# Optimization experiments

Measured on AMD Instinct MI355X. Metric: run time of the kernel, lower is better.

Reference implementation:

```python
import jax, jax.numpy as jnp
import numpy as np
import math

EMBED_DIM = 1024
NUM_HEADS = 16
HEAD_DIM = EMBED_DIM // NUM_HEADS
BATCH = 2
SEQ = 2048


def setup_inputs() -> dict:
    key = jax.random.key(0)
    ks = jax.random.split(key, 9)
    s = 1.0 / math.sqrt(EMBED_DIM)
    return {
        "x": jax.random.normal(ks[0], (BATCH, SEQ, EMBED_DIM), jnp.float32),
        "Wq": jax.random.normal(ks[1], (EMBED_DIM, EMBED_DIM), jnp.float32) * s,
        "bq": jnp.zeros((EMBED_DIM,), jnp.float32),
        "Wk": jax.random.normal(ks[2], (EMBED_DIM, EMBED_DIM), jnp.float32) * s,
        "bk": jnp.zeros((EMBED_DIM,), jnp.float32),
        "Wv": jax.random.normal(ks[3], (EMBED_DIM, EMBED_DIM), jnp.float32) * s,
        "bv": jnp.zeros((EMBED_DIM,), jnp.float32),
        "Wo": jax.random.normal(ks[4], (EMBED_DIM, EMBED_DIM), jnp.float32) * s,
        "bo": jnp.zeros((EMBED_DIM,), jnp.float32),
    }


def _rope_tables(seq_len, dim, dtype):
    inv_freq = 1.0 / (10000.0 ** (jnp.arange(0, dim, 2, dtype=jnp.float32) / dim))
    t = jnp.arange(seq_len, dtype=jnp.float32)
    freqs = jnp.einsum("i,j->ij", t, inv_freq)          # [S, D/2]
    emb = jnp.concatenate([freqs, freqs], axis=-1)       # [S, D]
    return jnp.cos(emb).astype(dtype), jnp.sin(emb).astype(dtype)


def _rotate_half(x):
    x1, x2 = jnp.split(x, 2, axis=-1)
    return jnp.concatenate([-x2, x1], axis=-1)


def _apply_rope(x, cos, sin):
    # x: [B, S, H, D]; cos/sin: [S, D] -> broadcast over batch & heads
    cos = cos[None, :, None, :]
    sin = sin[None, :, None, :]
    return x * cos + _rotate_half(x) * sin


def reference(x, Wq, bq, Wk, bk, Wv, bv, Wo, bo):
    B, S, E = x.shape
    H, D = NUM_HEADS, HEAD_DIM
    q = (x @ Wq + bq).reshape(B, S, H, D)
    k = (x @ Wk + bk).reshape(B, S, H, D)
    v = (x @ Wv + bv).reshape(B, S, H, D)
    cos, sin = _rope_tables(S, D, x.dtype)
    q = _apply_rope(q, cos, sin)
    k = _apply_rope(k, cos, sin)
    scale = 1.0 / math.sqrt(D)
    # scores: [B, H, S, S]
    scores = jnp.einsum("bqhd,bkhd->bhqk", q, k) * scale
    attn = jax.nn.softmax(scores, axis=-1)
    ctx = jnp.einsum("bhqk,bkhd->bqhd", attn, v).reshape(B, S, E)
    return ctx @ Wo + bo
```

## Files before the change

kernel.cpp:

```cpp
#include <hip/hip_runtime.h>
#include <math.h>

#define B_ 2
#define S_ 2048
#define E_ 1024
#define H_ 16
#define D_ 64
#define M_ (B_*S_)

typedef _Float16 f16x8  __attribute__((ext_vector_type(8)));
typedef _Float16 f16x4v __attribute__((ext_vector_type(4)));
typedef __fp16   h16x2  __attribute__((ext_vector_type(2)));
typedef float    f32x4  __attribute__((ext_vector_type(4)));

__device__ __forceinline__ ushort f2h(float f) {
    _Float16 h = (_Float16)f;
    return __builtin_bit_cast(ushort, h);
}

__device__ __forceinline__ void gload_lds16(const ushort* g, ushort* l) {
    __builtin_amdgcn_global_load_lds(
        (const __attribute__((address_space(1))) unsigned int*)g,
        (__attribute__((address_space(3))) unsigned int*)l, 16, 0, 0);
}

__device__ __forceinline__ float exp2_fast(float x) {
    return __builtin_amdgcn_exp2f(x);
}

__global__ void prep_kernel(const float* __restrict__ x,
                            const float* __restrict__ W0, const float* __restrict__ W1,
                            const float* __restrict__ W2, const float* __restrict__ W3,
                            ushort* __restrict__ xf, ushort* __restrict__ WT,
                            float* __restrict__ ct, float* __restrict__ st)
{
    const int bid = blockIdx.x;
    const int tid = threadIdx.x;
    __shared__ float tile[32][33];

    if (bid < 4096) {
        const int z = bid >> 10, rem = bid & 1023;
        const int k0 = (rem >> 5) * 32, nb = (rem & 31) * 32;
        const float* W = (z == 0) ? W0 : (z == 1) ? W1 : (z == 2) ? W2 : W3;
        const size_t zoff = (size_t)z * E_ * E_;
        const int tx = tid & 31, ty = tid >> 5;
        #pragma unroll
        for (int i = 0; i < 4; i++) {
            int r = i * 8 + ty;
            tile[r][tx] = W[(size_t)(k0 + r) * E_ + nb + tx];
        }
        __syncthreads();
        #pragma unroll
        for (int i = 0; i < 4; i++) {
            int r = i * 8 + ty;
            WT[zoff + (size_t)(nb + r) * E_ + k0 + tx] = f2h(tile[tx][r]);
        }
    } else if (bid < 8192) {
        const int i = (bid - 4096) * 1024 + tid * 4;
        float4 v = *(const float4*)&x[i];
        *(ushort4*)&xf[i] = make_ushort4(f2h(v.x), f2h(v.y), f2h(v.z), f2h(v.w));
    } else {
        const int i = (bid - 8192) * 256 + tid;
        const int j = i & 31, pos = i >> 5;
        float invf = (float)pow(10000.0, -(double)j / 32.0);
        float ang  = (float)pos * invf;
        ct[i] = (float)cos((double)ang);
        st[i] = (float)sin((double)ang);
    }
}

#define GBM 128
#define GBN 128
#define GBK 32
#define LOG2E 1.44269504088896340736f

__global__ __launch_bounds__(256, 3)
void gemm_f16(const ushort* __restrict__ A, const ushort* __restrict__ WTp,
              const float* __restrict__ b0, const float* __restrict__ b1,
              const float* __restrict__ b2,
              const float* __restrict__ ct, const float* __restrict__ st,
              ushort* __restrict__ outQ, ushort* __restrict__ outK,
              ushort* __restrict__ outV, float* __restrict__ outF,
              int force_mode)
{
    __shared__ __align__(16) ushort lA[2][GBM * GBK];
    __shared__ __align__(16) ushort lB[2][GBN * GBK];

    const int tid  = threadIdx.x;
    const int wv   = tid >> 6, lane = tid & 63;
    const int c    = lane & 15, qd = lane >> 4;
    const int rh   = wv >> 1, chn = wv & 1;

    const int mode = (force_mode >= 0) ? force_mode : (int)blockIdx.z;
    const size_t zoff = (force_mode >= 0) ? 0 : (size_t)blockIdx.z * (E_ * E_);
    const ushort* Bt = WTp + zoff;

    const int m0 = (blockIdx.x & 31) * GBM;
    const int n0 = (blockIdx.x >> 5) * GBN;

    const ushort* gsrc = (wv < 2) ? A : Bt;
    const int rowbase = ((wv < 2) ? m0 : n0) + (wv & 1) * 64;
    const int lofs = (wv & 1) * 64 * GBK;
    const int srow = lane >> 2;
    const int soct = (lane & 3) * 8;

    f32x4 acc[4][4] = {};

    #pragma unroll
    for (int cc = 0; cc < 4; cc++) {
        const ushort* g = gsrc + (size_t)(rowbase + cc * 16 + srow) * E_ + soct;
        gload_lds16(g, ((wv < 2) ? &lA[0][0] : &lB[0][0]) + lofs + cc * 512);
    }
    __syncthreads();

    for (int t = 0; t < E_ / GBK; t++) {
        if (t < E_ / GBK - 1) {
            const int nb = (t + 1) & 1;
            const int k0i = (t + 1) * GBK;
            ushort* dst = ((wv < 2) ? &lA[nb][0] : &lB[nb][0]) + lofs;
            #pragma unroll
            for (int cc = 0; cc < 4; cc++) {
                const ushort* g = gsrc + (size_t)(rowbase + cc * 16 + srow) * E_ + k0i + soct;
                gload_lds16(g, dst + cc * 512);
            }
        }

        const ushort* Ab = lA[t & 1];
        const ushort* Bb = lB[t & 1];

        f16x8 af[4], bf[4];
        #pragma unroll
        for (int mt = 0; mt < 4; mt++)
            af[mt] = *(const f16x8*)&Ab[(rh * 64 + mt * 16 + c) * GBK + qd * 8];
        #pragma unroll
        for (int nt = 0; nt < 4; nt++)
            bf[nt] = *(const f16x8*)&Bb[(chn * 64 + nt * 16 + c) * GBK + qd * 8];
        #pragma unroll
        for (int mt = 0; mt < 4; mt++)
            #pragma unroll
            for (int nt = 0; nt < 4; nt++)
                acc[mt][nt] = __builtin_amdgcn_mfma_f32_16x16x32_f16(af[mt], bf[nt], acc[mt][nt], 0, 0, 0);
        __syncthreads();
    }

    const float* bias = (mode == 0) ? b0 : (mode == 1) ? b1 : (mode == 2) ? b2 : b0;
    const int colbase = n0 + chn * 64;

    if (mode == 3) {
        #pragma unroll
        for (int mt = 0; mt < 4; mt++)
            #pragma unroll
            for (int r = 0; r < 4; r++) {
                const int row = m0 + rh * 64 + mt * 16 + qd * 4 + r;
                #pragma unroll
                for (int nt = 0; nt < 4; nt++) {
                    const int col = colbase + nt * 16 + c;
                    outF[(size_t)row * E_ + col] = acc[mt][nt][r] + bias[col];
                }
            }
    } else if (mode == 2) {
        const int hd = colbase >> 6;
        #pragma unroll
        for (int mt = 0; mt < 4; mt++)
            #pragma unroll
            for (int r = 0; r < 4; r++) {
                const int row = m0 + rh * 64 + mt * 16 + qd * 4 + r;
                const int bb = row >> 11, sl = row & (S_ - 1);
                const int tt = sl >> 7, key = sl & 127;
                const int c4 = key >> 2, inner = key & 3;
                const size_t base = (size_t)(bb * H_ + hd) * (S_ * D_) + tt * 8192;
                #pragma unroll
                for (int nt = 0; nt < 4; nt++) {
                    const int d = nt * 16 + c;
                    outV[base + d * 128 + ((c4 ^ (d & 7)) * 4) + inner]
                        = f2h(acc[mt][nt][r] + bias[colbase + d]);
                }
            }
    } else {
        ushort* O = (mode == 0) ? outQ : outK;
        const float sc = (mode == 0) ? 0.125f * LOG2E : 1.0f;
        #pragma unroll
        for (int mt = 0; mt < 4; mt++)
            #pragma unroll
            for (int r = 0; r < 4; r++) {
                const int row = m0 + rh * 64 + mt * 16 + qd * 4 + r;
                const int pos = row & (S_ - 1);
                const int sw = row & 7;
                #pragma unroll
                for (int p = 0; p < 2; p++) {
                    const int j32 = p * 16 + c;
                    const float cth = ct[pos * 32 + j32], sth = st[pos * 32 + j32];
                    const float v1 = acc[mt][p][r]     + bias[colbase + p * 16 + c];
                    const float v2 = acc[mt][p + 2][r] + bias[colbase + (p + 2) * 16 + c];
                    const float o1 = (v1 * cth - v2 * sth) * sc;
                    const float o2 = (v2 * cth + v1 * sth) * sc;
                    const int cd1 = p * 16 + c, cd2 = cd1 + 32;
                    O[(size_t)row * E_ + colbase + (((cd1 >> 3) ^ sw) * 8) + (cd1 & 7)] = f2h(o1);
                    O[(size_t)row * E_ + colbase + (((cd2 >> 3) ^ sw) * 8) + (cd2 & 7)] = f2h(o2);
                }
            }
    }
}

__global__ __launch_bounds__(256, 3)
void attn_mfma(const ushort* __restrict__ Qf, const ushort* __restrict__ Kf,
               const ushort* __restrict__ Vfg, ushort* __restrict__ ctxf)
{
    __shared__ __align__(16) ushort Kls[2][64 * 64];
    __shared__ __align__(16) ushort Vls[2][64 * 64];

    const int tid = threadIdx.x;
    const int wv = tid >> 6, lane = tid & 63;
    const int c = lane & 15, qd = lane >> 4;
    const int cs = c & 7;

    const int xcd = blockIdx.x & 7, ii = blockIdx.x >> 3;
    const int bh = xcd * 4 + (ii & 3);
    const int qtb = ii >> 2;
    const int b = bh >> 4, h = bh & 15;
    const int q0 = qtb * 64;

    const size_t qrow0 = (size_t)b * S_ + q0;
    const size_t krow0 = (size_t)b * S_;
    const size_t vbase = (size_t)bh * (S_ * D_);

    const int l8 = lane >> 3, l7 = lane & 7;

    #pragma unroll
    for (int j = 0; j < 2; j++) {
        const int row = wv * 16 + j * 8 + l8;
        gload_lds16(Qf + (qrow0 + row) * E_ + h * 64 + l7 * 8,
                    &Kls[0][wv * 1024 + j * 512]);
    }
    __syncthreads();
    f16x8 qfrag[4][2];
    #pragma unroll
    for (int qt = 0; qt < 4; qt++)
        #pragma unroll
        for (int kc = 0; kc < 2; kc++)
            qfrag[qt][kc] = *(const f16x8*)&Kls[0][(qt * 16 + c) * 64 + (((kc * 4 + qd) ^ cs) * 8)];
    __syncthreads();

    f32x4 acc[4][4] = {};
    float lsum[4] = {0.f, 0.f, 0.f, 0.f};

    if (wv < 2) {
        #pragma unroll
        for (int j = 0; j < 4; j++) {
            const int row = wv * 32 + j * 8 + l8;
            gload_lds16(Kf + (krow0 + row) * E_ + h * 64 + l7 * 8,
                        &Kls[0][wv * 2048 + j * 512]);
        }
    } else {
        #pragma unroll
        for (int j = 0; j < 4; j++) {
            const int drow = (wv - 2) * 32 + j * 8 + l8;
            gload_lds16(Vfg + vbase + drow * 128 + l7 * 8,
                        &Vls[0][(wv - 2) * 2048 + j * 512]);
        }
    }
    __syncthreads();

    #pragma unroll 1
    for (int t = 0; t < 32; t++) {
        if (t < 31) {
            const int nb = (t + 1) & 1;
            const int k0n = (t + 1) * 64;
            const int tt = (t + 1) >> 1, half = (t + 1) & 1;
            if (wv < 2) {
                #pragma unroll
                for (int j = 0; j < 4; j++) {
                    const int row = wv * 32 + j * 8 + l8;
                    gload_lds16(Kf + (krow0 + k0n + row) * E_ + h * 64 + l7 * 8,
                                &Kls[nb][wv * 2048 + j * 512]);
                }
            } else {
                #pragma unroll
                for (int j = 0; j < 4; j++) {
                    const int drow = (wv - 2) * 32 + j * 8 + l8;
                    gload_lds16(Vfg + vbase + tt * 8192 + drow * 128 + half * 64 + l7 * 8,
                                &Vls[nb][(wv - 2) * 2048 + j * 512]);
                }
            }
        }

        const ushort* kb = Kls[t & 1];
        const ushort* vb = Vls[t & 1];

        f16x8 kfr[2];
        #pragma unroll
        for (int kc = 0; kc < 2; kc++)
            kfr[kc] = *(const f16x8*)&kb[(wv * 16 + c) * 64 + (((kc * 4 + qd) ^ cs) * 8)];

        f16x4v bfrag[4];
        #pragma unroll
        for (int qt = 0; qt < 4; qt++) {
            f32x4 s = {};
            s = __builtin_amdgcn_mfma_f32_16x16x32_f16(kfr[0], qfrag[qt][0], s, 0, 0, 0);
            s = __builtin_amdgcn_mfma_f32_16x16x32_f16(kfr[1], qfrag[qt][1], s, 0, 0, 0);
            const float p0 = exp2_fast(s[0]), p1 = exp2_fast(s[1]);
            const float p2 = exp2_fast(s[2]), p3 = exp2_fast(s[3]);
            lsum[qt] += (p0 + p1) + (p2 + p3);
            h16x2 lo = __builtin_amdgcn_cvt_pkrtz(p0, p1);
            h16x2 hi = __builtin_amdgcn_cvt_pkrtz(p2, p3);
            uint2 u;
            u.x = __builtin_bit_cast(unsigned int, lo);
            u.y = __builtin_bit_cast(unsigned int, hi);
            bfrag[qt] = __builtin_bit_cast(f16x4v, u);
        }

        #pragma unroll
        for (int dt = 0; dt < 4; dt++) {
            f16x4v vfr = *(const f16x4v*)&vb[(dt * 16 + c) * 64 + (((wv * 4 + qd) ^ cs) * 4)];
            #pragma unroll
            for (int qt = 0; qt < 4; qt++)
                acc[dt][qt] = __builtin_amdgcn_mfma_f32_16x16x16f16(vfr, bfrag[qt], acc[dt][qt], 0, 0, 0);
        }
        __syncthreads();
    }

    float* red = (float*)&Kls[0][0];
    float* lsr = (float*)&Vls[0][0];

    #pragma unroll
    for (int qt = 0; qt < 4; qt++) {
        float v = lsum[qt];
        v += __shfl_xor(v, 16);
        v += __shfl_xor(v, 32);
        lsum[qt] = v;
    }
    if (lane < 16) {
        #pragma unroll
        for (int qt = 0; qt < 4; qt++) lsr[wv * 64 + qt * 16 + lane] = lsum[qt];
    }

    f32x4 own[4];
    #pragma unroll
    for (int qt = 0; qt < 4; qt++)
        own[qt] = (wv == 0) ? acc[0][qt] : (wv == 1) ? acc[1][qt]
                : (wv == 2) ? acc[2][qt] : acc[3][qt];

    #pragma unroll
    for (int r = 1; r < 4; r++) {
        const int ds = (wv + r) & 3;
        #pragma unroll
        for (int qt = 0; qt < 4; qt++) {
            f32x4 sv = (ds == 0) ? acc[0][qt] : (ds == 1) ? acc[1][qt]
                     : (ds == 2) ? acc[2][qt] : acc[3][qt];
            *(f32x4*)&red[ds * 1024 + qt * 256 + lane * 4] = sv;
        }
        __syncthreads();
        #pragma unroll
        for (int qt = 0; qt < 4; qt++)
            own[qt] += *(const f32x4*)&red[wv * 1024 + qt * 256 + lane * 4];
        if (r < 3) __syncthreads();
    }

    float inv[4];
    #pragma unroll
    for (int qt = 0; qt < 4; qt++) {
        const int q = qt * 16 + c;
        inv[qt] = 1.0f / (lsr[q] + lsr[64 + q] + lsr[128 + q] + lsr[192 + q]);
    }

    const size_t obase = qrow0 * E_ + h * 64 + wv * 16 + qd * 4;
    #pragma unroll
    for (int qt = 0; qt < 4; qt++) {
        f32x4 v = own[qt];
        const float iq = inv[qt];
        ushort4 o = make_ushort4(f2h(v[0] * iq), f2h(v[1] * iq),
                                 f2h(v[2] * iq), f2h(v[3] * iq));
        *(ushort4*)&ctxf[obase + (size_t)(qt * 16 + c) * E_] = o;
    }
}

extern "C" void kernel_launch(void* const* d_in, const int* in_sizes, int n_in,
                              void* d_out, int out_size, void* d_ws, size_t ws_size,
                              hipStream_t stream)
{
    const float* x  = (const float*)d_in[0];
    const float* Wq = (const float*)d_in[1];
    const float* bq = (const float*)d_in[2];
    const float* Wk = (const float*)d_in[3];
    const float* bk = (const float*)d_in[4];
    const float* Wv = (const float*)d_in[5];
    const float* bv = (const float*)d_in[6];
    const float* Wo = (const float*)d_in[7];
    const float* bo = (const float*)d_in[8];
    float* out = (float*)d_out;

    ushort* Qb = (ushort*)d_ws;
    ushort* Kb = Qb + (size_t)M_ * E_;
    ushort* Vf = Kb + (size_t)M_ * E_;
    ushort* xf = Vf + (size_t)M_ * E_;
    ushort* WT = xf + (size_t)M_ * E_;
    float*  ct = (float*)(WT + (size_t)4 * E_ * E_);
    float*  st = ct + S_ * 32;
    ushort* ctxf = Qb;

    hipLaunchKernelGGL(prep_kernel, dim3(8448), dim3(256), 0, stream,
                       x, Wq, Wk, Wv, Wo, xf, WT, ct, st);

    hipLaunchKernelGGL(gemm_f16, dim3(256, 1, 3), dim3(256), 0, stream,
                       xf, WT, bq, bk, bv, ct, st,
                       Qb, Kb, Vf, (float*)nullptr, -1);

    hipLaunchKernelGGL(attn_mfma, dim3(B_ * H_ * (S_ / 64)), dim3(256), 0, stream,
                       Qb, Kb, Vf, ctxf);

    hipLaunchKernelGGL(gemm_f16, dim3(256), dim3(256), 0, stream,
                       ctxf, WT + (size_t)3 * E_ * E_, bo, bo, bo, ct, st,
                       (ushort*)nullptr, (ushort*)nullptr, (ushort*)nullptr, out, 3);
}
```

Baseline: 200.5 us.

## Give each wave private K/V LDS slices and drop per-tile block barriers

Result: faster. 195.4 us (-2.6%).

```diff
diff --git a/kernel.cpp b/kernel.cpp
--- a/kernel.cpp
+++ b/kernel.cpp
@@ -166,14 +166,12 @@
             for (int r = 0; r < 4; r++) {
                 const int row = m0 + rh * 64 + mt * 16 + qd * 4 + r;
                 const int bb = row >> 11, sl = row & (S_ - 1);
-                const int tt = sl >> 7, key = sl & 127;
-                const int c4 = key >> 2, inner = key & 3;
-                const size_t base = (size_t)(bb * H_ + hd) * (S_ * D_) + tt * 8192;
+                const size_t base = (size_t)(bb * H_ + hd) * (S_ * D_)
+                                  + (sl >> 6) * 4096 + ((sl >> 4) & 3) * 1024 + (sl & 15);
                 #pragma unroll
                 for (int nt = 0; nt < 4; nt++) {
                     const int d = nt * 16 + c;
-                    outV[base + d * 128 + ((c4 ^ (d & 7)) * 4) + inner]
-                        = f2h(acc[mt][nt][r] + bias[colbase + d]);
+                    outV[base + d * 16] = f2h(acc[mt][nt][r] + bias[colbase + d]);
                 }
             }
     } else {
@@ -206,8 +204,7 @@
 void attn_mfma(const ushort* __restrict__ Qf, const ushort* __restrict__ Kf,
                const ushort* __restrict__ Vfg, ushort* __restrict__ ctxf)
 {
-    __shared__ __align__(16) ushort Kls[2][64 * 64];
-    __shared__ __align__(16) ushort Vls[2][64 * 64];
+    __shared__ __align__(16) ushort L[16384];
 
     const int tid = threadIdx.x;
     const int wv = tid >> 6, lane = tid & 63;
@@ -229,8 +226,7 @@
     #pragma unroll
     for (int j = 0; j < 2; j++) {
         const int row = wv * 16 + j * 8 + l8;
-        gload_lds16(Qf + (qrow0 + row) * E_ + h * 64 + l7 * 8,
-                    &Kls[0][wv * 1024 + j * 512]);
+        gload_lds16(Qf + (qrow0 + row) * E_ + h * 64 + l7 * 8, &L[wv * 1024 + j * 512]);
     }
     __syncthreads();
     f16x8 qfrag[4][2];
@@ -238,59 +234,48 @@
     for (int qt = 0; qt < 4; qt++)
         #pragma unroll
         for (int kc = 0; kc < 2; kc++)
-            qfrag[qt][kc] = *(const f16x8*)&Kls[0][(qt * 16 + c) * 64 + (((kc * 4 + qd) ^ cs) * 8)];
+            qfrag[qt][kc] = *(const f16x8*)&L[(qt * 16 + c) * 64 + (((kc * 4 + qd) ^ cs) * 8)];
     __syncthreads();
 
     f32x4 acc[4][4] = {};
     float lsum[4] = {0.f, 0.f, 0.f, 0.f};
 
-    if (wv < 2) {
-        #pragma unroll
-        for (int j = 0; j < 4; j++) {
-            const int row = wv * 32 + j * 8 + l8;
-            gload_lds16(Kf + (krow0 + row) * E_ + h * 64 + l7 * 8,
-                        &Kls[0][wv * 2048 + j * 512]);
-        }
-    } else {
-        #pragma unroll
-        for (int j = 0; j < 4; j++) {
-            const int drow = (wv - 2) * 32 + j * 8 + l8;
-            gload_lds16(Vfg + vbase + drow * 128 + l7 * 8,
-                        &Vls[0][(wv - 2) * 2048 + j * 512]);
-        }
-    }
-    __syncthreads();
+    ushort* const myL = &L[wv * 4096];
+
+    #pragma unroll
+    for (int j = 0; j < 2; j++)
+        gload_lds16(Kf + (krow0 + wv * 16 + j * 8 + l8) * E_ + h * 64 + l7 * 8,
+                    myL + j * 512);
+    #pragma unroll
+    for (int j = 0; j < 2; j++)
+        gload_lds16(Vfg + vbase + wv * 1024 + j * 512 + lane * 8,
+                    myL + 1024 + j * 512);
 
     #pragma unroll 1
     for (int t = 0; t < 32; t++) {
         if (t < 31) {
-            const int nb = (t + 1) & 1;
+            ushort* nb = myL + ((t + 1) & 1) * 2048;
             const int k0n = (t + 1) * 64;
-            const int tt = (t + 1) >> 1, half = (t + 1) & 1;
-            if (wv < 2) {
-                #pragma unroll
-                for (int j = 0; j < 4; j++) {
-                    const int row = wv * 32 + j * 8 + l8;
-                    gload_lds16(Kf + (krow0 + k0n + row) * E_ + h * 64 + l7 * 8,
-                                &Kls[nb][wv * 2048 + j * 512]);
-                }
-            } else {
-                #pragma unroll
-                for (int j = 0; j < 4; j++) {
-                    const int drow = (wv - 2) * 32 + j * 8 + l8;
-                    gload_lds16(Vfg + vbase + tt * 8192 + drow * 128 + half * 64 + l7 * 8,
-                                &Vls[nb][(wv - 2) * 2048 + j * 512]);
-                }
-            }
-        }
-
-        const ushort* kb = Kls[t & 1];
-        const ushort* vb = Vls[t & 1];
+            #pragma unroll
+            for (int j = 0; j < 2; j++)
+                gload_lds16(Kf + (krow0 + k0n + wv * 16 + j * 8 + l8) * E_ + h * 64 + l7 * 8,
+                            nb + j * 512);
+            #pragma unroll
+            for (int j = 0; j < 2; j++)
+                gload_lds16(Vfg + vbase + (t + 1) * 4096 + wv * 1024 + j * 512 + lane * 8,
+                            nb + 1024 + j * 512);
+            __builtin_amdgcn_s_waitcnt(0x0F74);
+        } else {
+            __builtin_amdgcn_s_waitcnt(0x0F70);
+        }
+
+        const ushort* kb = myL + (t & 1) * 2048;
+        const ushort* vb = kb + 1024;
 
         f16x8 kfr[2];
         #pragma unroll
         for (int kc = 0; kc < 2; kc++)
-            kfr[kc] = *(const f16x8*)&kb[(wv * 16 + c) * 64 + (((kc * 4 + qd) ^ cs) * 8)];
+            kfr[kc] = *(const f16x8*)&kb[c * 64 + (((kc * 4 + qd) ^ cs) * 8)];
 
         f16x4v bfrag[4];
         #pragma unroll
@@ -311,16 +296,17 @@
 
         #pragma unroll
         for (int dt = 0; dt < 4; dt++) {
-            f16x4v vfr = *(const f16x4v*)&vb[(dt * 16 + c) * 64 + (((wv * 4 + qd) ^ cs) * 4)];
+            f16x4v vfr = *(const f16x4v*)&vb[(dt * 16 + c) * 16 + qd * 4];
             #pragma unroll
             for (int qt = 0; qt < 4; qt++)
                 acc[dt][qt] = __builtin_amdgcn_mfma_f32_16x16x16f16(vfr, bfrag[qt], acc[dt][qt], 0, 0, 0);
         }
-        __syncthreads();
-    }
-
-    float* red = (float*)&Kls[0][0];
-    float* lsr = (float*)&Vls[0][0];
+    }
+
+    __syncthreads();
+
+    float* red = (float*)&L[0];
+    float* lsr = (float*)&L[8192];
 
     #pragma unroll
     for (int qt = 0; qt < 4; qt++) {
```
